# Kernel optimization log

Hardware: AMD Instinct MI355X
Metric: run time of the kernel (lower is better)

The kernel has to match this reference:

```python
import jax, jax.numpy as jnp
import numpy as np

SOFTCLAMP = 50.0
CAUSAL_BLOCK = 256      # causal_block_size (tokens per time block)
NUM_SPECIAL = 8         # num_special_tokens
SPECIAL_SEQ = 2048      # block_size_per_special (defaults to kv seq len)
ROPE_BASE = 10000.0


def setup_inputs() -> dict:
    key = jax.random.key(0)
    kq, kk, kv = jax.random.split(key, 3)
    b, h, hk, s, d = 2, 16, 4, 2048, 64
    q = jax.random.normal(kq, (b, h, s, d), dtype=jnp.float32)
    k = jax.random.normal(kk, (b, hk, s, d), dtype=jnp.float32)
    v = jax.random.normal(kv, (b, hk, s, d), dtype=jnp.float32)
    # standard 1D rotary angles: [seq, dim_head]
    inv_freq = 1.0 / (ROPE_BASE ** (jnp.arange(0, d, 2, dtype=jnp.float32) / d))
    freqs = jnp.arange(s, dtype=jnp.float32)[:, None] * inv_freq[None, :]  # [s, d/2]
    rotations = jnp.concatenate((freqs, freqs), axis=-1)                   # [s, d]
    return {"q": q, "k": k, "v": v, "rotations": rotations}


def _apply_rotations(rotations, t):
    # t: [b, h, s, d]; rotations: [s, d] (broadcast over batch/heads)
    x1, x2 = jnp.split(t, 2, axis=-1)
    rotated_half = jnp.concatenate((-x2, x1), axis=-1)
    return t * jnp.cos(rotations) + rotated_half * jnp.sin(rotations)


def _forward(q, k, v, rotations):
    b, h, i, d = q.shape
    hk, j = k.shape[1], k.shape[2]
    scale = d ** -0.5
    q = _apply_rotations(rotations[:i], q)
    k = _apply_rotations(rotations[:j], k)
    g = h // hk  # GQA groups
    qg = q.reshape(b, hk, g, i, d)
    sim = jnp.einsum('bhgid,bhjd->bhgij', qg, k) * scale
    # softclamp score mod
    sim = jnp.tanh(sim / SOFTCLAMP) * SOFTCLAMP
    # special-token mask (faithful to source: compares raw q/k indices)
    qi = jnp.arange(i)[:, None]
    kj = jnp.arange(j)[None, :]
    special_start = SPECIAL_SEQ - NUM_SPECIAL
    q_is_special = qi >= special_start
    k_is_special = kj >= special_start
    special_mask = ~(~q_is_special & k_is_special)  # non-special q cannot see special k
    # block-causal mask: allowed when query block >= key block
    causal_allow = (qi // CAUSAL_BLOCK) >= (kj // CAUSAL_BLOCK)
    allow = special_mask & causal_allow  # [i, j], broadcasts over b,h,g
    mask_value = -jnp.finfo(sim.dtype).max
    sim = jnp.where(allow, sim, mask_value)
    attn = jax.nn.softmax(sim, axis=-1)
    out = jnp.einsum('bhgij,bhjd->bhgid', attn, v)
    return out.reshape(b, h, i, d)


def reference(q, k, v, rotations):
    return _forward(q, k, v, rotations)
```

## Files before the change

### kernel.cpp

```cpp
#include <hip/hip_runtime.h>
#include <stdint.h>

typedef unsigned short u16;
typedef short s16x8 __attribute__((ext_vector_type(8)));
typedef float f32x4 __attribute__((ext_vector_type(4)));

#define SQ 2048
#define DH 64
#define BN 64
#define STR 72
#define SPECIAL_START 2040
#define NBH 32
#define NKV 8
#define NQP 16
#define NITEMS (NBH * NQP)
#define ATTN_GRID 512
#define K1F  0.18033688011112043f
#define KPAF 4.9244826e-9f
#define KPBF -6.406040185576019e-5f
#define KEF  36.067376022224085f

union U8 { s16x8 v; short e[8]; };
union F4 { f32x4 v; float e[4]; };

__device__ __forceinline__ u16 f2bf(float x) {
    uint32_t u = __float_as_uint(x);
    return (u16)((u + 0x7fffu + ((u >> 16) & 1u)) >> 16);
}
__device__ __forceinline__ uint32_t pkbf(float a, float b) {
    uint32_t r;
    asm("v_cvt_pk_bf16_f32 %0, %1, %2" : "=v"(r) : "v"(a), "v"(b));
    return r;
}
__device__ __forceinline__ float exp2hw(float x) {
    float r; asm("v_exp_f32 %0, %1" : "=v"(r) : "v"(x)); return r;
}
__device__ __forceinline__ float2 fsincos(float ang) {
    float r = ang * 0.15915494309189535f;
    r -= floorf(r);
    float s, c;
    asm("v_sin_f32 %0, %1" : "=v"(s) : "v"(r));
    asm("v_cos_f32 %0, %1" : "=v"(c) : "v"(r));
    return make_float2(s, c);
}
__device__ __forceinline__ void gl_lds16(const void* g, void* l) {
    __builtin_amdgcn_global_load_lds(
        (const __attribute__((address_space(1))) uint32_t*)g,
        (__attribute__((address_space(3))) uint32_t*)l, 16, 0, 0);
}

#define VTILES (NKV * 32)
#define RK (NKV * SQ)
#define KBLK (RK / 32)
__global__ __launch_bounds__(256)
void prep_kernel(const float* __restrict__ kg, const float* __restrict__ vg,
                 const float* __restrict__ rotg,
                 u16* __restrict__ kp, u16* __restrict__ vp,
                 uint32_t* __restrict__ cnt)
{
    const int tid = threadIdx.x;
    if (blockIdx.x == 0 && tid == 0) *cnt = 0u;
    if (blockIdx.x < VTILES) {
        __shared__ short Vls[64 * STR];
        const int tile = blockIdx.x;
        const float* src = vg + ((size_t)(tile >> 5) * SQ + (size_t)(tile & 31) * 64) * DH;
        {
            int kv = tid >> 2, c0 = (tid & 3) * 16;
            const float* s4 = src + (size_t)kv * DH + c0;
            float4 f0 = *(const float4*)(s4);
            float4 f1 = *(const float4*)(s4 + 4);
            float4 f2 = *(const float4*)(s4 + 8);
            float4 f3 = *(const float4*)(s4 + 12);
            uint4 w0 = make_uint4(pkbf(f0.x, f0.y), pkbf(f0.z, f0.w),
                                  pkbf(f1.x, f1.y), pkbf(f1.z, f1.w));
            uint4 w1 = make_uint4(pkbf(f2.x, f2.y), pkbf(f2.z, f2.w),
                                  pkbf(f3.x, f3.y), pkbf(f3.z, f3.w));
            *(uint4*)&Vls[kv * STR + c0]     = w0;
            *(uint4*)&Vls[kv * STR + c0 + 8] = w1;
        }
        __syncthreads();
        {
            int d = tid >> 2, c0 = (tid & 3) * 16;
            U8 o0, o1;
#pragma unroll
            for (int j = 0; j < 16; j++)
                (j < 8 ? o0 : o1).e[j & 7] = Vls[(c0 + j) * STR + d];
            u16* dst = vp + (((size_t)tile * 64 + d) << 6) + c0;
            *(s16x8*)dst       = o0.v;
            *(s16x8*)(dst + 8) = o1.v;
        }
    } else {
        int bx = blockIdx.x - VTILES;
        int r8 = tid >> 3, c0 = (tid & 7) * 4;
        int r = bx * 32 + r8;
        const int s = r & (SQ - 1);
        const float* src = kg + (size_t)r * DH;
        u16*         dst = kp + (size_t)r * DH;
        float4 a  = *(const float4*)(src + c0);
        float4 b  = *(const float4*)(src + c0 + 32);
        float4 rv = *(const float4*)(rotg + (size_t)s * DH + c0);
        float2 s0 = fsincos(rv.x), s1 = fsincos(rv.y),
               s2 = fsincos(rv.z), s3 = fsincos(rv.w);
        float lo0 = a.x * s0.y - b.x * s0.x, hi0 = b.x * s0.y + a.x * s0.x;
        float lo1 = a.y * s1.y - b.y * s1.x, hi1 = b.y * s1.y + a.y * s1.x;
        float lo2 = a.z * s2.y - b.z * s2.x, hi2 = b.z * s2.y + a.z * s2.x;
        float lo3 = a.w * s3.y - b.w * s3.x, hi3 = b.w * s3.y + a.w * s3.x;
        *(uint2*)(dst + c0)      = make_uint2(pkbf(lo0, lo1), pkbf(lo2, lo3));
        *(uint2*)(dst + c0 + 32) = make_uint2(pkbf(hi0, hi1), pkbf(hi2, hi3));
    }
}

__global__ __launch_bounds__(256)
__attribute__((amdgpu_waves_per_eu(3, 4)))
void attn_fast(const float* __restrict__ qg, const float* __restrict__ rotg,
               const u16* __restrict__ kp, const u16* __restrict__ vp,
               uint32_t* __restrict__ cnt, float* __restrict__ outg)
{
    const int tid = threadIdx.x;
    const int wv = tid >> 6, lane = tid & 63;
    const int l15 = lane & 15, quad = lane >> 4;
    const int swl = (l15 & 7) << 3;

    __shared__ __align__(16) u16 Ks[2][4096];
    __shared__ __align__(16) u16 Vt[2][4096];
    __shared__ __align__(16) short Ps[128 * 64];
    __shared__ int s_w;

    const int gcol = (((lane & 7) ^ (lane >> 3)) << 3);
    const int goff0 = ((wv * 16 + (lane >> 3)) << 6) + gcol;
    const int goff1 = goff0 + (8 << 6);
    const int lds0 = (wv * 2) * 512;
    const int lds1 = lds0 + 512;

    short* prow0 = &Ps[(wv * 32 + l15) * 64];
    short* prow1 = &Ps[(wv * 32 + 16 + l15) * 64];

    for (;;) {
        __syncthreads();
        if (tid == 0) s_w = (int)atomicAdd(cnt, 1u);
        __syncthreads();
        const int w = s_w;
        if (w >= NITEMS) break;
        const int qp = (NQP - 1) - (w >> 5);
        const int u  = w & 31, bkv = u >> 2;
        const int bh = ((bkv >> 2) << 4) | ((bkv & 3) << 2) | (u & 3);
        const int nkt = (((qp >> 1) + 1)) << 2;
        const int qrow0 = qp * 128 + wv * 32;

        const u16* kbase = kp + (size_t)bkv * (SQ * DH);
        const u16* vbase = vp + (size_t)bkv * (SQ * DH);
        auto stage = [&](int kt, int cb) {
            const u16* tk = kbase + ((size_t)kt << 12);
            const u16* tv = vbase + ((size_t)kt << 12);
            gl_lds16(tk + goff0, &Ks[cb][lds0]);
            gl_lds16(tk + goff1, &Ks[cb][lds1]);
            gl_lds16(tv + goff0, &Vt[cb][lds0]);
            gl_lds16(tv + goff1, &Vt[cb][lds1]);
        };
        stage(0, 0);

        s16x8 qf[2][2];
#pragma unroll
        for (int nq = 0; nq < 2; nq++) {
            const int srow = qrow0 + nq * 16 + l15;
            const float* gq = qg + ((size_t)bh * SQ + srow) * DH + quad * 8;
            float a[8], b[8];
            *(float4*)&a[0] = *(const float4*)(gq);
            *(float4*)&a[4] = *(const float4*)(gq + 4);
            *(float4*)&b[0] = *(const float4*)(gq + 32);
            *(float4*)&b[4] = *(const float4*)(gq + 36);
            const float* rrow = rotg + (size_t)srow * DH + quad * 8;
            float lo[8], hi[8];
#pragma unroll
            for (int j = 0; j < 8; j++) {
                float2 sc = fsincos(rrow[j]);
                lo[j] = a[j] * sc.y - b[j] * sc.x;
                hi[j] = b[j] * sc.y + a[j] * sc.x;
            }
            U8 q0, q1;
#pragma unroll
            for (int j = 0; j < 4; j++) {
                ((uint32_t*)&q0.v)[j] = pkbf(lo[2 * j], lo[2 * j + 1]);
                ((uint32_t*)&q1.v)[j] = pkbf(hi[2 * j], hi[2 * j + 1]);
            }
            qf[nq][0] = q0.v;
            qf[nq][1] = q1.v;
        }

        F4 oa[2][4];
#pragma unroll
        for (int nq = 0; nq < 2; nq++)
#pragma unroll
            for (int mb = 0; mb < 4; mb++) oa[nq][mb].v = (f32x4){0.f, 0.f, 0.f, 0.f};
        F4 lsa0, lsa1;
        lsa0.v = (f32x4){0.f, 0.f, 0.f, 0.f};
        lsa1.v = (f32x4){0.f, 0.f, 0.f, 0.f};

        __syncthreads();
        int cb = 0;

        for (int kt = 0; kt < nkt; kt++) {
            if (kt + 1 < nkt) stage(kt + 1, cb ^ 1);

            F4 sa[2][4];
            __builtin_amdgcn_s_setprio(1);
#pragma unroll
            for (int ks = 0; ks < 2; ks++)
#pragma unroll
                for (int mb = 0; mb < 4; mb++) {
                    s16x8 kf = *(const s16x8*)&Ks[cb][(mb * 16 + l15) * 64 + ((ks * 32 + quad * 8) ^ swl)];
                    sa[0][mb].v = __builtin_amdgcn_mfma_f32_16x16x32_bf16(
                        kf, qf[0][ks], ks ? sa[0][mb].v : (f32x4){0.f, 0.f, 0.f, 0.f}, 0, 0, 0);
                    sa[1][mb].v = __builtin_amdgcn_mfma_f32_16x16x32_bf16(
                        kf, qf[1][ks], ks ? sa[1][mb].v : (f32x4){0.f, 0.f, 0.f, 0.f}, 0, 0, 0);
                }
            __builtin_amdgcn_s_setprio(0);

            const int last = (kt == 31);
#pragma unroll
            for (int nq = 0; nq < 2; nq++) {
                const int qglob = qrow0 + nq * 16 + l15;
                short* prow = nq ? prow1 : prow0;
#pragma unroll
                for (int mb = 0; mb < 4; mb++) {
                    F4 t, w2, py, pa;
                    t.v  = sa[nq][mb].v * K1F;
                    w2.v = t.v * t.v;
                    py.v = w2.v * KPAF + KPBF;
                    py.v = w2.v * py.v + 1.0f;
                    t.v  = t.v * py.v - KEF;
                    pa.e[0] = exp2hw(t.e[0]);
                    pa.e[1] = exp2hw(t.e[1]);
                    pa.e[2] = exp2hw(t.e[2]);
                    pa.e[3] = exp2hw(t.e[3]);
                    if (last && qglob < SPECIAL_START) {
#pragma unroll
                        for (int c = 0; c < 4; c++) {
                            int kvglob = kt * BN + mb * 16 + quad * 4 + c;
                            if (kvglob >= SPECIAL_START) pa.e[c] = 0.f;
                        }
                    }
                    if (nq) lsa1.v = lsa1.v + pa.v; else lsa0.v = lsa0.v + pa.v;
                    uint2 pw = make_uint2(pkbf(pa.e[0], pa.e[1]),
                                          pkbf(pa.e[2], pa.e[3]));
                    *(uint2*)&prow[(mb * 16 + quad * 4) ^ swl] = pw;
                }
            }

            s16x8 pf00 = *(const s16x8*)&prow0[(quad * 8) ^ swl];
            s16x8 pf01 = *(const s16x8*)&prow0[(32 + quad * 8) ^ swl];
            s16x8 pf10 = *(const s16x8*)&prow1[(quad * 8) ^ swl];
            s16x8 pf11 = *(const s16x8*)&prow1[(32 + quad * 8) ^ swl];
            __builtin_amdgcn_s_setprio(1);
#pragma unroll
            for (int mb = 0; mb < 4; mb++) {
                s16x8 vf = *(const s16x8*)&Vt[cb][(mb * 16 + l15) * 64 + ((quad * 8) ^ swl)];
                oa[0][mb].v = __builtin_amdgcn_mfma_f32_16x16x32_bf16(vf, pf00, oa[0][mb].v, 0, 0, 0);
                oa[1][mb].v = __builtin_amdgcn_mfma_f32_16x16x32_bf16(vf, pf10, oa[1][mb].v, 0, 0, 0);
            }
#pragma unroll
            for (int mb = 0; mb < 4; mb++) {
                s16x8 vf = *(const s16x8*)&Vt[cb][(mb * 16 + l15) * 64 + ((32 + quad * 8) ^ swl)];
                oa[0][mb].v = __builtin_amdgcn_mfma_f32_16x16x32_bf16(vf, pf01, oa[0][mb].v, 0, 0, 0);
                oa[1][mb].v = __builtin_amdgcn_mfma_f32_16x16x32_bf16(vf, pf11, oa[1][mb].v, 0, 0, 0);
            }
            __builtin_amdgcn_s_setprio(0);

            __syncthreads();
            cb ^= 1;
        }

        float lsum0 = (lsa0.e[0] + lsa0.e[1]) + (lsa0.e[2] + lsa0.e[3]);
        float lsum1 = (lsa1.e[0] + lsa1.e[1]) + (lsa1.e[2] + lsa1.e[3]);
        lsum0 += __shfl_xor(lsum0, 16, 64);
        lsum0 += __shfl_xor(lsum0, 32, 64);
        lsum1 += __shfl_xor(lsum1, 16, 64);
        lsum1 += __shfl_xor(lsum1, 32, 64);

#pragma unroll
        for (int nq = 0; nq < 2; nq++) {
            const float rl = 1.0f / (nq ? lsum1 : lsum0);
            const int qrow = qrow0 + nq * 16 + l15;
            float* orow = outg + ((size_t)bh * SQ + qrow) * DH;
#pragma unroll
            for (int mb = 0; mb < 4; mb++) {
                const int d0 = mb * 16 + quad * 4;
                const F4& o = oa[nq][mb];
                *(float4*)(orow + d0) = make_float4(o.e[0] * rl, o.e[1] * rl,
                                                    o.e[2] * rl, o.e[3] * rl);
            }
        }
    }
}

__global__ __launch_bounds__(256, 4)
void attn_fallback(const float* __restrict__ qg, const float* __restrict__ kg,
                   const float* __restrict__ vg, const float* __restrict__ rotg,
                   float* __restrict__ outg)
{
    const int x  = blockIdx.x;
    const int qt = (x & 1) ? (31 - (x >> 1)) : (x >> 1);
    const int bh = blockIdx.y;
    const int bb = bh >> 4, hh = bh & 15;
    const int bkv = bb * 4 + (hh >> 2);
    const int qs = qt * 64;

    const int tid = threadIdx.x;
    const int wv = tid >> 6, lane = tid & 63;
    const int l15 = lane & 15, quad = lane >> 4;
    const int swl = (l15 & 7) << 3;

    __shared__ __align__(16) short QPs[64 * 64];
    __shared__ __align__(16) short Ks[2][BN * 64];
    __shared__ __align__(16) short Vt[2][DH * 64];

    const size_t kvbase = ((size_t)bkv * SQ) * DH;
    const int nkt = (qt / 4 + 1) * 4;
    const int qglob = qs + wv * 16 + l15;

    {
        int rr = tid >> 2, c0 = (tid & 3) * 8;
        int srow = qs + rr;
        const float* gq = qg + ((size_t)bh * SQ + srow) * DH;
        float a[8], b[8];
        *(float4*)&a[0] = *(const float4*)(gq + c0);
        *(float4*)&a[4] = *(const float4*)(gq + c0 + 4);
        *(float4*)&b[0] = *(const float4*)(gq + c0 + 32);
        *(float4*)&b[4] = *(const float4*)(gq + c0 + 36);
        U8 o0, o1;
#pragma unroll
        for (int j = 0; j < 8; j++) {
            float2 sc = fsincos(rotg[(size_t)srow * DH + c0 + j]);
            o0.e[j] = (short)f2bf(a[j] * sc.y - b[j] * sc.x);
            o1.e[j] = (short)f2bf(b[j] * sc.y + a[j] * sc.x);
        }
        int sw2 = (rr & 7) << 3;
        *(s16x8*)&QPs[rr * 64 + (c0 ^ sw2)]        = o0.v;
        *(s16x8*)&QPs[rr * 64 + ((c0 + 32) ^ sw2)] = o1.v;
    }
    __syncthreads();

    s16x8 qf[2];
#pragma unroll
    for (int ks = 0; ks < 2; ks++)
        qf[ks] = *(const s16x8*)&QPs[(wv * 16 + l15) * 64 + ((ks * 32 + quad * 8) ^ swl)];

    F4 oa[4];
#pragma unroll
    for (int mb = 0; mb < 4; mb++) oa[mb].v = (f32x4){0.f, 0.f, 0.f, 0.f};
    float lsum = 0.f;

    for (int kt = 0; kt < nkt; kt++) {
        const int cb = kt & 1;
        {
            int rr = tid >> 2, c0 = (tid & 3) * 8;
            int srow = kt * BN + rr;
            const float* gk = kg + kvbase + (size_t)srow * DH;
            float a[8], b[8];
            *(float4*)&a[0] = *(const float4*)(gk + c0);
            *(float4*)&a[4] = *(const float4*)(gk + c0 + 4);
            *(float4*)&b[0] = *(const float4*)(gk + c0 + 32);
            *(float4*)&b[4] = *(const float4*)(gk + c0 + 36);
            U8 o0, o1;
#pragma unroll
            for (int j = 0; j < 8; j++) {
                float2 sc = fsincos(rotg[(size_t)(srow & (SQ - 1)) * DH + c0 + j]);
                o0.e[j] = (short)f2bf(a[j] * sc.y - b[j] * sc.x);
                o1.e[j] = (short)f2bf(b[j] * sc.y + a[j] * sc.x);
            }
            int sw2 = (rr & 7) << 3;
            *(s16x8*)&Ks[cb][rr * 64 + (c0 ^ sw2)]        = o0.v;
            *(s16x8*)&Ks[cb][rr * 64 + ((c0 + 32) ^ sw2)] = o1.v;
        }
        {
            int rr = tid >> 2, c0 = (tid & 3) * 16;
            const float* gv = vg + kvbase + (size_t)(kt * BN + rr) * DH;
            float vv[16];
#pragma unroll
            for (int t = 0; t < 4; t++)
                *(float4*)&vv[t * 4] = *(const float4*)(gv + c0 + t * 4);
#pragma unroll
            for (int j = 0; j < 16; j++) {
                int d = c0 + j;
                Vt[cb][d * 64 + (rr ^ ((d & 7) << 3))] = (short)f2bf(vv[j]);
            }
        }
        __syncthreads();

        F4 sa[4];
#pragma unroll
        for (int mb = 0; mb < 4; mb++) sa[mb].v = (f32x4){0.f, 0.f, 0.f, 0.f};
#pragma unroll
        for (int ks = 0; ks < 2; ks++)
#pragma unroll
            for (int mb = 0; mb < 4; mb++) {
                s16x8 kf = *(const s16x8*)&Ks[cb][(mb * 16 + l15) * 64 + ((ks * 32 + quad * 8) ^ swl)];
                sa[mb].v = __builtin_amdgcn_mfma_f32_16x16x32_bf16(kf, qf[ks], sa[mb].v, 0, 0, 0);
            }

        F4 pa[4];
#pragma unroll
        for (int mb = 0; mb < 4; mb++)
#pragma unroll
            for (int c = 0; c < 4; c++) {
                float t  = sa[mb].e[c] * K1F;
                float w2 = t * t;
                float poly = fmaf(w2, fmaf(w2, KPAF, KPBF), 1.0f);
                pa[mb].e[c] = exp2hw(fmaf(t, poly, -KEF));
            }
        if (kt == 31 && qglob < SPECIAL_START) {
#pragma unroll
            for (int mb = 0; mb < 4; mb++)
#pragma unroll
                for (int c = 0; c < 4; c++) {
                    int kvglob = kt * BN + mb * 16 + quad * 4 + c;
                    if (kvglob >= SPECIAL_START) pa[mb].e[c] = 0.f;
                }
        }
        short* prow = &QPs[(wv * 16 + l15) * 64];
#pragma unroll
        for (int mb = 0; mb < 4; mb++) {
            lsum += (pa[mb].e[0] + pa[mb].e[1]) + (pa[mb].e[2] + pa[mb].e[3]);
            uint2 pw = make_uint2(pkbf(pa[mb].e[0], pa[mb].e[1]),
                                  pkbf(pa[mb].e[2], pa[mb].e[3]));
            *(uint2*)&prow[(mb * 16 + quad * 4) ^ swl] = pw;
        }
#pragma unroll
        for (int ks = 0; ks < 2; ks++) {
            s16x8 pf = *(const s16x8*)&prow[(ks * 32 + quad * 8) ^ swl];
#pragma unroll
            for (int mb = 0; mb < 4; mb++) {
                s16x8 vf = *(const s16x8*)&Vt[cb][(mb * 16 + l15) * 64 + ((ks * 32 + quad * 8) ^ swl)];
                oa[mb].v = __builtin_amdgcn_mfma_f32_16x16x32_bf16(vf, pf, oa[mb].v, 0, 0, 0);
            }
        }
        __syncthreads();
    }

    lsum += __shfl_xor(lsum, 16, 64);
    lsum += __shfl_xor(lsum, 32, 64);

    float rl = 1.0f / lsum;
    int qrow = qs + wv * 16 + l15;
    float* orow = outg + ((size_t)bh * SQ + qrow) * DH;
#pragma unroll
    for (int mb = 0; mb < 4; mb++) {
        int d0 = mb * 16 + quad * 4;
        *(float4*)(orow + d0) = make_float4(oa[mb].e[0] * rl, oa[mb].e[1] * rl,
                                            oa[mb].e[2] * rl, oa[mb].e[3] * rl);
    }
}

extern "C" void kernel_launch(void* const* d_in, const int* in_sizes, int n_in,
                              void* d_out, int out_size, void* d_ws, size_t ws_size,
                              hipStream_t stream) {
    const float* q   = (const float*)d_in[0];
    const float* k   = (const float*)d_in[1];
    const float* v   = (const float*)d_in[2];
    const float* rot = (const float*)d_in[3];
    float* out = (float*)d_out;

    char* w = (char*)d_ws;
    const size_t k_bytes = (size_t)NKV * SQ * DH * sizeof(u16);
    const size_t v_bytes = k_bytes;
    u16* kp = (u16*)w;
    u16* vp = (u16*)(w + k_bytes);
    uint32_t* cnt = (uint32_t*)(w + k_bytes + v_bytes);

    if (ws_size >= k_bytes + v_bytes + sizeof(uint32_t)) {
        hipLaunchKernelGGL(prep_kernel, dim3(VTILES + KBLK), dim3(256), 0, stream,
                           k, v, rot, kp, vp, cnt);
        hipLaunchKernelGGL(attn_fast, dim3(ATTN_GRID), dim3(256), 0, stream,
                           q, rot, kp, vp, cnt, out);
    } else {
        hipLaunchKernelGGL(attn_fallback, dim3(32, NBH), dim3(256), 0, stream,
                           q, k, v, rot, out);
    }
}
```

Measured before the change: 129.7 us.

## Split long causal query blocks across KV chunks with a separate reduce pass

Work items are now (query-block, KV-range) chunks of up to 8 key tiles, listed in a static table, instead of whole query blocks with variable lengths up to 32 tiles. Each chunk writes unnormalized partial outputs and row sums to workspace, and a new reduce kernel sums the chunks per query block and normalizes. The aim is better load balance and less tail idle time over 768 persistent blocks. In exchange it adds a partial-result write and read through global memory plus an extra kernel launch. The old single-pass kernel is kept as a fallback for small workspaces.

```diff
diff --git a/kernel.cpp b/kernel.cpp
--- a/kernel.cpp
+++ b/kernel.cpp
@@ -13,8 +13,11 @@
 #define NBH 32
 #define NKV 8
 #define NQP 16
-#define NITEMS (NBH * NQP)
-#define ATTN_GRID 512
+#define NCLS 40
+#define NITEMS_F (NCLS * 32)
+#define ATTN_GRID_F 768
+#define NITEMS_M (NBH * NQP)
+#define ATTN_GRID_M 512
 #define K1F  0.18033688011112043f
 #define KPAF 4.9244826e-9f
 #define KPBF -6.406040185576019e-5f
@@ -22,6 +25,32 @@
 
 union U8 { s16x8 v; short e[8]; };
 union F4 { f32x4 v; float e[4]; };
+
+#define CL(qp,k0,nk) ((unsigned short)((qp) | ((k0) << 4) | ((nk) << 9)))
+__device__ const unsigned short ETAB[NCLS] = {
+    CL(15,0,8), CL(15,8,8), CL(15,16,8), CL(15,24,8),
+    CL(14,0,8), CL(14,8,8), CL(14,16,8), CL(14,24,8),
+    CL(13,0,8), CL(13,8,8), CL(13,16,8),
+    CL(12,0,8), CL(12,8,8), CL(12,16,8),
+    CL(11,0,8), CL(11,8,8), CL(11,16,8),
+    CL(10,0,8), CL(10,8,8), CL(10,16,8),
+    CL(9,0,8),  CL(9,8,8),
+    CL(8,0,8),  CL(8,8,8),
+    CL(7,0,8),  CL(7,8,8),
+    CL(6,0,8),  CL(6,8,8),
+    CL(5,0,8),
+    CL(4,0,8),
+    CL(3,0,8),
+    CL(2,0,8),
+    CL(13,24,4), CL(12,24,4), CL(9,16,4), CL(8,16,4),
+    CL(5,8,4),   CL(4,8,4),   CL(1,0,4),  CL(0,0,4)
+};
+__device__ const signed char QPS[16][4] = {
+    {39,-1,-1,-1}, {38,-1,-1,-1}, {31,-1,-1,-1}, {30,-1,-1,-1},
+    {29,37,-1,-1}, {28,36,-1,-1}, {26,27,-1,-1}, {24,25,-1,-1},
+    {22,23,35,-1}, {20,21,34,-1}, {17,18,19,-1}, {14,15,16,-1},
+    {11,12,13,33}, {8,9,10,32},   {4,5,6,7},     {0,1,2,3}
+};
 
 __device__ __forceinline__ u16 f2bf(float x) {
     uint32_t u = __float_as_uint(x);
@@ -114,7 +143,8 @@
 __attribute__((amdgpu_waves_per_eu(3, 4)))
 void attn_fast(const float* __restrict__ qg, const float* __restrict__ rotg,
                const u16* __restrict__ kp, const u16* __restrict__ vp,
-               uint32_t* __restrict__ cnt, float* __restrict__ outg)
+               uint32_t* __restrict__ cnt,
+               float* __restrict__ pacc, float* __restrict__ lacc)
 {
     const int tid = threadIdx.x;
     const int wv = tid >> 6, lane = tid & 63;
@@ -140,11 +170,14 @@
         if (tid == 0) s_w = (int)atomicAdd(cnt, 1u);
         __syncthreads();
         const int w = s_w;
-        if (w >= NITEMS) break;
-        const int qp = (NQP - 1) - (w >> 5);
-        const int u  = w & 31, bkv = u >> 2;
+        if (w >= NITEMS_F) break;
+        const int g = w >> 5;
+        const int u = w & 31, bkv = u >> 2;
         const int bh = ((bkv >> 2) << 4) | ((bkv & 3) << 2) | (u & 3);
-        const int nkt = (((qp >> 1) + 1)) << 2;
+        const int e = ETAB[g];
+        const int qp  = e & 15;
+        const int kt0 = (e >> 4) & 31;
+        const int nk  = e >> 9;
         const int qrow0 = qp * 128 + wv * 32;
 
         const u16* kbase = kp + (size_t)bkv * (SQ * DH);
@@ -157,7 +190,7 @@
             gl_lds16(tv + goff0, &Vt[cb][lds0]);
             gl_lds16(tv + goff1, &Vt[cb][lds1]);
         };
-        stage(0, 0);
+        stage(kt0, 0);
 
         s16x8 qf[2][2];
 #pragma unroll
@@ -199,8 +232,9 @@
         __syncthreads();
         int cb = 0;
 
-        for (int kt = 0; kt < nkt; kt++) {
-            if (kt + 1 < nkt) stage(kt + 1, cb ^ 1);
+        for (int i = 0; i < nk; i++) {
+            const int kt = kt0 + i;
+            if (i + 1 < nk) stage(kt + 1, cb ^ 1);
 
             F4 sa[2][4];
             __builtin_amdgcn_s_setprio(1);
@@ -277,6 +311,229 @@
         lsum1 += __shfl_xor(lsum1, 16, 64);
         lsum1 += __shfl_xor(lsum1, 32, 64);
 
+        float* pitem = pacc + (size_t)w * 8192;
+        float* litem = lacc + (size_t)w * 128;
+#pragma unroll
+        for (int nq = 0; nq < 2; nq++) {
+            const int row = wv * 32 + nq * 16 + l15;
+#pragma unroll
+            for (int mb = 0; mb < 4; mb++) {
+                const F4& o = oa[nq][mb];
+                *(float4*)&pitem[row * 64 + mb * 16 + quad * 4] =
+                    make_float4(o.e[0], o.e[1], o.e[2], o.e[3]);
+            }
+            if (quad == 0) litem[row] = nq ? lsum1 : lsum0;
+        }
+    }
+}
+
+__global__ __launch_bounds__(256)
+void reduce_kernel(const float* __restrict__ pacc, const float* __restrict__ lacc,
+                   float* __restrict__ outg)
+{
+    const int blk = blockIdx.x;
+    const int bh = blk >> 4, qp = blk & 15;
+    const int t = threadIdx.x;
+    const int row = t >> 1;
+    const int c0 = (t & 1) * 32;
+    const int bkv = (bh >> 4) * 4 + ((bh >> 2) & 3);
+    const int u = (bkv << 2) | (bh & 3);
+
+    float acc[32];
+#pragma unroll
+    for (int j = 0; j < 32; j++) acc[j] = 0.f;
+    float ls = 0.f;
+#pragma unroll
+    for (int s = 0; s < 4; s++) {
+        const int g = QPS[qp][s];
+        if (g < 0) break;
+        const int id = g * 32 + u;
+        const float* p = pacc + (size_t)id * 8192 + row * 64 + c0;
+#pragma unroll
+        for (int j = 0; j < 8; j++) {
+            float4 v = ((const float4*)p)[j];
+            acc[4 * j]     += v.x;
+            acc[4 * j + 1] += v.y;
+            acc[4 * j + 2] += v.z;
+            acc[4 * j + 3] += v.w;
+        }
+        ls += lacc[(size_t)id * 128 + row];
+    }
+    const float rl = 1.0f / ls;
+    float* orow = outg + ((size_t)bh * SQ + qp * 128 + row) * DH + c0;
+#pragma unroll
+    for (int j = 0; j < 8; j++)
+        ((float4*)orow)[j] = make_float4(acc[4 * j] * rl, acc[4 * j + 1] * rl,
+                                         acc[4 * j + 2] * rl, acc[4 * j + 3] * rl);
+}
+
+__global__ __launch_bounds__(256)
+__attribute__((amdgpu_waves_per_eu(3, 4)))
+void attn_mid(const float* __restrict__ qg, const float* __restrict__ rotg,
+              const u16* __restrict__ kp, const u16* __restrict__ vp,
+              uint32_t* __restrict__ cnt, float* __restrict__ outg)
+{
+    const int tid = threadIdx.x;
+    const int wv = tid >> 6, lane = tid & 63;
+    const int l15 = lane & 15, quad = lane >> 4;
+    const int swl = (l15 & 7) << 3;
+
+    __shared__ __align__(16) u16 Ks[2][4096];
+    __shared__ __align__(16) u16 Vt[2][4096];
+    __shared__ __align__(16) short Ps[128 * 64];
+    __shared__ int s_w;
+
+    const int gcol = (((lane & 7) ^ (lane >> 3)) << 3);
+    const int goff0 = ((wv * 16 + (lane >> 3)) << 6) + gcol;
+    const int goff1 = goff0 + (8 << 6);
+    const int lds0 = (wv * 2) * 512;
+    const int lds1 = lds0 + 512;
+
+    short* prow0 = &Ps[(wv * 32 + l15) * 64];
+    short* prow1 = &Ps[(wv * 32 + 16 + l15) * 64];
+
+    for (;;) {
+        __syncthreads();
+        if (tid == 0) s_w = (int)atomicAdd(cnt, 1u);
+        __syncthreads();
+        const int w = s_w;
+        if (w >= NITEMS_M) break;
+        const int qp = (NQP - 1) - (w >> 5);
+        const int u  = w & 31, bkv = u >> 2;
+        const int bh = ((bkv >> 2) << 4) | ((bkv & 3) << 2) | (u & 3);
+        const int nkt = (((qp >> 1) + 1)) << 2;
+        const int qrow0 = qp * 128 + wv * 32;
+
+        const u16* kbase = kp + (size_t)bkv * (SQ * DH);
+        const u16* vbase = vp + (size_t)bkv * (SQ * DH);
+        auto stage = [&](int kt, int cb) {
+            const u16* tk = kbase + ((size_t)kt << 12);
+            const u16* tv = vbase + ((size_t)kt << 12);
+            gl_lds16(tk + goff0, &Ks[cb][lds0]);
+            gl_lds16(tk + goff1, &Ks[cb][lds1]);
+            gl_lds16(tv + goff0, &Vt[cb][lds0]);
+            gl_lds16(tv + goff1, &Vt[cb][lds1]);
+        };
+        stage(0, 0);
+
+        s16x8 qf[2][2];
+#pragma unroll
+        for (int nq = 0; nq < 2; nq++) {
+            const int srow = qrow0 + nq * 16 + l15;
+            const float* gq = qg + ((size_t)bh * SQ + srow) * DH + quad * 8;
+            float a[8], b[8];
+            *(float4*)&a[0] = *(const float4*)(gq);
+            *(float4*)&a[4] = *(const float4*)(gq + 4);
+            *(float4*)&b[0] = *(const float4*)(gq + 32);
+            *(float4*)&b[4] = *(const float4*)(gq + 36);
+            const float* rrow = rotg + (size_t)srow * DH + quad * 8;
+            float lo[8], hi[8];
+#pragma unroll
+            for (int j = 0; j < 8; j++) {
+                float2 sc = fsincos(rrow[j]);
+                lo[j] = a[j] * sc.y - b[j] * sc.x;
+                hi[j] = b[j] * sc.y + a[j] * sc.x;
+            }
+            U8 q0, q1;
+#pragma unroll
+            for (int j = 0; j < 4; j++) {
+                ((uint32_t*)&q0.v)[j] = pkbf(lo[2 * j], lo[2 * j + 1]);
+                ((uint32_t*)&q1.v)[j] = pkbf(hi[2 * j], hi[2 * j + 1]);
+            }
+            qf[nq][0] = q0.v;
+            qf[nq][1] = q1.v;
+        }
+
+        F4 oa[2][4];
+#pragma unroll
+        for (int nq = 0; nq < 2; nq++)
+#pragma unroll
+            for (int mb = 0; mb < 4; mb++) oa[nq][mb].v = (f32x4){0.f, 0.f, 0.f, 0.f};
+        F4 lsa0, lsa1;
+        lsa0.v = (f32x4){0.f, 0.f, 0.f, 0.f};
+        lsa1.v = (f32x4){0.f, 0.f, 0.f, 0.f};
+
+        __syncthreads();
+        int cb = 0;
+
+        for (int kt = 0; kt < nkt; kt++) {
+            if (kt + 1 < nkt) stage(kt + 1, cb ^ 1);
+
+            F4 sa[2][4];
+            __builtin_amdgcn_s_setprio(1);
+#pragma unroll
+            for (int ks = 0; ks < 2; ks++)
+#pragma unroll
+                for (int mb = 0; mb < 4; mb++) {
+                    s16x8 kf = *(const s16x8*)&Ks[cb][(mb * 16 + l15) * 64 + ((ks * 32 + quad * 8) ^ swl)];
+                    sa[0][mb].v = __builtin_amdgcn_mfma_f32_16x16x32_bf16(
+                        kf, qf[0][ks], ks ? sa[0][mb].v : (f32x4){0.f, 0.f, 0.f, 0.f}, 0, 0, 0);
+                    sa[1][mb].v = __builtin_amdgcn_mfma_f32_16x16x32_bf16(
+                        kf, qf[1][ks], ks ? sa[1][mb].v : (f32x4){0.f, 0.f, 0.f, 0.f}, 0, 0, 0);
+                }
+            __builtin_amdgcn_s_setprio(0);
+
+            const int last = (kt == 31);
+#pragma unroll
+            for (int nq = 0; nq < 2; nq++) {
+                const int qglob = qrow0 + nq * 16 + l15;
+                short* prow = nq ? prow1 : prow0;
+#pragma unroll
+                for (int mb = 0; mb < 4; mb++) {
+                    F4 t, w2, py, pa;
+                    t.v  = sa[nq][mb].v * K1F;
+                    w2.v = t.v * t.v;
+                    py.v = w2.v * KPAF + KPBF;
+                    py.v = w2.v * py.v + 1.0f;
+                    t.v  = t.v * py.v - KEF;
+                    pa.e[0] = exp2hw(t.e[0]);
+                    pa.e[1] = exp2hw(t.e[1]);
+                    pa.e[2] = exp2hw(t.e[2]);
+                    pa.e[3] = exp2hw(t.e[3]);
+                    if (last && qglob < SPECIAL_START) {
+#pragma unroll
+                        for (int c = 0; c < 4; c++) {
+                            int kvglob = kt * BN + mb * 16 + quad * 4 + c;
+                            if (kvglob >= SPECIAL_START) pa.e[c] = 0.f;
+                        }
+                    }
+                    if (nq) lsa1.v = lsa1.v + pa.v; else lsa0.v = lsa0.v + pa.v;
+                    uint2 pw = make_uint2(pkbf(pa.e[0], pa.e[1]),
+                                          pkbf(pa.e[2], pa.e[3]));
+                    *(uint2*)&prow[(mb * 16 + quad * 4) ^ swl] = pw;
+                }
+            }
+
+            s16x8 pf00 = *(const s16x8*)&prow0[(quad * 8) ^ swl];
+            s16x8 pf01 = *(const s16x8*)&prow0[(32 + quad * 8) ^ swl];
+            s16x8 pf10 = *(const s16x8*)&prow1[(quad * 8) ^ swl];
+            s16x8 pf11 = *(const s16x8*)&prow1[(32 + quad * 8) ^ swl];
+            __builtin_amdgcn_s_setprio(1);
+#pragma unroll
+            for (int mb = 0; mb < 4; mb++) {
+                s16x8 vf = *(const s16x8*)&Vt[cb][(mb * 16 + l15) * 64 + ((quad * 8) ^ swl)];
+                oa[0][mb].v = __builtin_amdgcn_mfma_f32_16x16x32_bf16(vf, pf00, oa[0][mb].v, 0, 0, 0);
+                oa[1][mb].v = __builtin_amdgcn_mfma_f32_16x16x32_bf16(vf, pf10, oa[1][mb].v, 0, 0, 0);
+            }
+#pragma unroll
+            for (int mb = 0; mb < 4; mb++) {
+                s16x8 vf = *(const s16x8*)&Vt[cb][(mb * 16 + l15) * 64 + ((32 + quad * 8) ^ swl)];
+                oa[0][mb].v = __builtin_amdgcn_mfma_f32_16x16x32_bf16(vf, pf01, oa[0][mb].v, 0, 0, 0);
+                oa[1][mb].v = __builtin_amdgcn_mfma_f32_16x16x32_bf16(vf, pf11, oa[1][mb].v, 0, 0, 0);
+            }
+            __builtin_amdgcn_s_setprio(0);
+
+            __syncthreads();
+            cb ^= 1;
+        }
+
+        float lsum0 = (lsa0.e[0] + lsa0.e[1]) + (lsa0.e[2] + lsa0.e[3]);
+        float lsum1 = (lsa1.e[0] + lsa1.e[1]) + (lsa1.e[2] + lsa1.e[3]);
+        lsum0 += __shfl_xor(lsum0, 16, 64);
+        lsum0 += __shfl_xor(lsum0, 32, 64);
+        lsum1 += __shfl_xor(lsum1, 16, 64);
+        lsum1 += __shfl_xor(lsum1, 32, 64);
+
 #pragma unroll
         for (int nq = 0; nq < 2; nq++) {
             const float rl = 1.0f / (nq ? lsum1 : lsum0);
@@ -463,14 +720,30 @@
     char* w = (char*)d_ws;
     const size_t k_bytes = (size_t)NKV * SQ * DH * sizeof(u16);
     const size_t v_bytes = k_bytes;
+    const size_t cnt_off = k_bytes + v_bytes;
+    const size_t pacc_off = cnt_off + 256;
+    const size_t pacc_bytes = (size_t)NITEMS_F * 8192 * sizeof(float);
+    const size_t lacc_off = pacc_off + pacc_bytes;
+    const size_t lacc_bytes = (size_t)NITEMS_F * 128 * sizeof(float);
+    const size_t full_need = lacc_off + lacc_bytes;
+
     u16* kp = (u16*)w;
     u16* vp = (u16*)(w + k_bytes);
-    uint32_t* cnt = (uint32_t*)(w + k_bytes + v_bytes);
-
-    if (ws_size >= k_bytes + v_bytes + sizeof(uint32_t)) {
+    uint32_t* cnt = (uint32_t*)(w + cnt_off);
+    float* pacc = (float*)(w + pacc_off);
+    float* lacc = (float*)(w + lacc_off);
+
+    if (ws_size >= full_need) {
         hipLaunchKernelGGL(prep_kernel, dim3(VTILES + KBLK), dim3(256), 0, stream,
                            k, v, rot, kp, vp, cnt);
-        hipLaunchKernelGGL(attn_fast, dim3(ATTN_GRID), dim3(256), 0, stream,
+        hipLaunchKernelGGL(attn_fast, dim3(ATTN_GRID_F), dim3(256), 0, stream,
+                           q, rot, kp, vp, cnt, pacc, lacc);
+        hipLaunchKernelGGL(reduce_kernel, dim3(NBH * NQP), dim3(256), 0, stream,
+                           pacc, lacc, out);
+    } else if (ws_size >= cnt_off + sizeof(uint32_t)) {
+        hipLaunchKernelGGL(prep_kernel, dim3(VTILES + KBLK), dim3(256), 0, stream,
+                           k, v, rot, kp, vp, cnt);
+        hipLaunchKernelGGL(attn_mid, dim3(ATTN_GRID_M), dim3(256), 0, stream,
                            q, rot, kp, vp, cnt, out);
     } else {
         hipLaunchKernelGGL(attn_fallback, dim3(32, NBH), dim3(256), 0, stream,
```

Measured after the change: 138.8 us. +7.0%, slower.

## Split long query rows across KV chunks with atomic-counted partial merge

Applied to the files above, without the earlier changes.

Work items are redefined through a static table that splits the longer causal query-block rows into chunks of eight key tiles. Partial unnormalised outputs and row sums go to workspace, and the last finisher per query block merges them through an atomic completion counter. V is re-laid out in the prep kernel so each lane loads its MFMA fragments straight from global memory into registers, double-buffered across iterations. This drops the V LDS buffers and allows a larger grid and lower occupancy floor. The aim is better load balance and shorter critical paths, at the cost of extra partial-result traffic, fences and more register pressure.

```diff
diff --git a/kernel.cpp b/kernel.cpp
--- a/kernel.cpp
+++ b/kernel.cpp
@@ -13,8 +13,9 @@
 #define NBH 32
 #define NKV 8
 #define NQP 16
-#define NITEMS (NBH * NQP)
-#define ATTN_GRID 512
+#define NCLS 40
+#define NITEMS_F (NCLS * 32)
+#define ATTN_GRID_F 768
 #define K1F  0.18033688011112043f
 #define KPAF 4.9244826e-9f
 #define KPBF -6.406040185576019e-5f
@@ -22,6 +23,32 @@
 
 union U8 { s16x8 v; short e[8]; };
 union F4 { f32x4 v; float e[4]; };
+
+#define CL(qp,k0,nk,ns) ((unsigned short)((qp) | ((k0) << 4) | ((nk) << 9) | ((ns) << 13)))
+__device__ const unsigned short ETAB[NCLS] = {
+    CL(15,0,8,4), CL(15,8,8,4), CL(15,16,8,4), CL(15,24,8,4),
+    CL(14,0,8,4), CL(14,8,8,4), CL(14,16,8,4), CL(14,24,8,4),
+    CL(13,0,8,4), CL(13,8,8,4), CL(13,16,8,4),
+    CL(12,0,8,4), CL(12,8,8,4), CL(12,16,8,4),
+    CL(11,0,8,3), CL(11,8,8,3), CL(11,16,8,3),
+    CL(10,0,8,3), CL(10,8,8,3), CL(10,16,8,3),
+    CL(9,0,8,3),  CL(9,8,8,3),
+    CL(8,0,8,3),  CL(8,8,8,3),
+    CL(7,0,8,2),  CL(7,8,8,2),
+    CL(6,0,8,2),  CL(6,8,8,2),
+    CL(5,0,8,2),
+    CL(4,0,8,2),
+    CL(3,0,8,1),
+    CL(2,0,8,1),
+    CL(13,24,4,4), CL(12,24,4,4), CL(9,16,4,3), CL(8,16,4,3),
+    CL(5,8,4,2),   CL(4,8,4,2),   CL(1,0,4,1),  CL(0,0,4,1)
+};
+__device__ const signed char QPS[16][4] = {
+    {39,-1,-1,-1}, {38,-1,-1,-1}, {31,-1,-1,-1}, {30,-1,-1,-1},
+    {29,37,-1,-1}, {28,36,-1,-1}, {26,27,-1,-1}, {24,25,-1,-1},
+    {22,23,35,-1}, {20,21,34,-1}, {17,18,19,-1}, {14,15,16,-1},
+    {11,12,13,33}, {8,9,10,32},   {4,5,6,7},     {0,1,2,3}
+};
 
 __device__ __forceinline__ u16 f2bf(float x) {
     uint32_t u = __float_as_uint(x);
@@ -56,10 +83,14 @@
 void prep_kernel(const float* __restrict__ kg, const float* __restrict__ vg,
                  const float* __restrict__ rotg,
                  u16* __restrict__ kp, u16* __restrict__ vp,
-                 uint32_t* __restrict__ cnt)
+                 uint32_t* __restrict__ cnt, uint32_t* __restrict__ done)
 {
     const int tid = threadIdx.x;
-    if (blockIdx.x == 0 && tid == 0) *cnt = 0u;
+    if (blockIdx.x == 0) {
+        if (tid == 0) *cnt = 0u;
+        done[tid] = 0u;
+        done[tid + 256] = 0u;
+    }
     if (blockIdx.x < VTILES) {
         __shared__ short Vls[64 * STR];
         const int tile = blockIdx.x;
@@ -85,9 +116,12 @@
 #pragma unroll
             for (int j = 0; j < 16; j++)
                 (j < 8 ? o0 : o1).e[j & 7] = Vls[(c0 + j) * STR + d];
-            u16* dst = vp + (((size_t)tile * 64 + d) << 6) + c0;
-            *(s16x8*)dst       = o0.v;
-            *(s16x8*)(dst + 8) = o1.v;
+            u16* dst = vp + (size_t)tile * 4096
+                          + ((size_t)((d >> 4) * 2 + (c0 >> 5))) * 512
+                          + (d & 15) * 8;
+            const int q0 = (c0 >> 3) & 3;
+            *(s16x8*)(dst + q0 * 128)       = o0.v;
+            *(s16x8*)(dst + (q0 + 1) * 128) = o1.v;
         }
     } else {
         int bx = blockIdx.x - VTILES;
@@ -111,10 +145,12 @@
 }
 
 __global__ __launch_bounds__(256)
-__attribute__((amdgpu_waves_per_eu(3, 4)))
+__attribute__((amdgpu_waves_per_eu(2, 4)))
 void attn_fast(const float* __restrict__ qg, const float* __restrict__ rotg,
                const u16* __restrict__ kp, const u16* __restrict__ vp,
-               uint32_t* __restrict__ cnt, float* __restrict__ outg)
+               uint32_t* __restrict__ cnt, uint32_t* __restrict__ done,
+               float* __restrict__ pacc, float* __restrict__ lacc,
+               float* __restrict__ outg)
 {
     const int tid = threadIdx.x;
     const int wv = tid >> 6, lane = tid & 63;
@@ -122,9 +158,8 @@
     const int swl = (l15 & 7) << 3;
 
     __shared__ __align__(16) u16 Ks[2][4096];
-    __shared__ __align__(16) u16 Vt[2][4096];
     __shared__ __align__(16) short Ps[128 * 64];
-    __shared__ int s_w;
+    __shared__ int s_w, s_d;
 
     const int gcol = (((lane & 7) ^ (lane >> 3)) << 3);
     const int goff0 = ((wv * 16 + (lane >> 3)) << 6) + gcol;
@@ -140,24 +175,33 @@
         if (tid == 0) s_w = (int)atomicAdd(cnt, 1u);
         __syncthreads();
         const int w = s_w;
-        if (w >= NITEMS) break;
-        const int qp = (NQP - 1) - (w >> 5);
-        const int u  = w & 31, bkv = u >> 2;
+        if (w >= NITEMS_F) break;
+        const int g = w >> 5;
+        const int u = w & 31, bkv = u >> 2;
         const int bh = ((bkv >> 2) << 4) | ((bkv & 3) << 2) | (u & 3);
-        const int nkt = (((qp >> 1) + 1)) << 2;
+        const int e = ETAB[g];
+        const int qp  = e & 15;
+        const int kt0 = (e >> 4) & 31;
+        const int nk  = (e >> 9) & 15;
+        const int nsl = e >> 13;
         const int qrow0 = qp * 128 + wv * 32;
 
         const u16* kbase = kp + (size_t)bkv * (SQ * DH);
-        const u16* vbase = vp + (size_t)bkv * (SQ * DH);
-        auto stage = [&](int kt, int cb) {
+        const u16* vbase = vp + ((size_t)(bkv * 32)) * 4096 + lane * 8;
+        auto stage_k = [&](int kt, int cb) {
             const u16* tk = kbase + ((size_t)kt << 12);
-            const u16* tv = vbase + ((size_t)kt << 12);
             gl_lds16(tk + goff0, &Ks[cb][lds0]);
             gl_lds16(tk + goff1, &Ks[cb][lds1]);
-            gl_lds16(tv + goff0, &Vt[cb][lds0]);
-            gl_lds16(tv + goff1, &Vt[cb][lds1]);
         };
-        stage(0, 0);
+        s16x8 vfA[8], vfB[8];
+        auto loadV = [&](s16x8 (&vf)[8], int kt) {
+            const u16* p = vbase + ((size_t)kt << 12);
+#pragma unroll
+            for (int f = 0; f < 8; f++)
+                vf[f] = *(const s16x8*)(p + f * 512);
+        };
+        stage_k(kt0, 0);
+        loadV(vfA, kt0);
 
         s16x8 qf[2][2];
 #pragma unroll
@@ -195,14 +239,9 @@
         F4 lsa0, lsa1;
         lsa0.v = (f32x4){0.f, 0.f, 0.f, 0.f};
         lsa1.v = (f32x4){0.f, 0.f, 0.f, 0.f};
-
-        __syncthreads();
-        int cb = 0;
-
-        for (int kt = 0; kt < nkt; kt++) {
-            if (kt + 1 < nkt) stage(kt + 1, cb ^ 1);
-
-            F4 sa[2][4];
+        F4 sa[2][4];
+
+        auto QK = [&](int cb) {
             __builtin_amdgcn_s_setprio(1);
 #pragma unroll
             for (int ks = 0; ks < 2; ks++)
@@ -215,7 +254,8 @@
                         kf, qf[1][ks], ks ? sa[1][mb].v : (f32x4){0.f, 0.f, 0.f, 0.f}, 0, 0, 0);
                 }
             __builtin_amdgcn_s_setprio(0);
-
+        };
+        auto SM = [&](int kt) {
             const int last = (kt == 31);
 #pragma unroll
             for (int nq = 0; nq < 2; nq++) {
@@ -246,7 +286,8 @@
                     *(uint2*)&prow[(mb * 16 + quad * 4) ^ swl] = pw;
                 }
             }
-
+        };
+        auto PV = [&](const s16x8 (&vf)[8]) {
             s16x8 pf00 = *(const s16x8*)&prow0[(quad * 8) ^ swl];
             s16x8 pf01 = *(const s16x8*)&prow0[(32 + quad * 8) ^ swl];
             s16x8 pf10 = *(const s16x8*)&prow1[(quad * 8) ^ swl];
@@ -254,20 +295,34 @@
             __builtin_amdgcn_s_setprio(1);
 #pragma unroll
             for (int mb = 0; mb < 4; mb++) {
-                s16x8 vf = *(const s16x8*)&Vt[cb][(mb * 16 + l15) * 64 + ((quad * 8) ^ swl)];
-                oa[0][mb].v = __builtin_amdgcn_mfma_f32_16x16x32_bf16(vf, pf00, oa[0][mb].v, 0, 0, 0);
-                oa[1][mb].v = __builtin_amdgcn_mfma_f32_16x16x32_bf16(vf, pf10, oa[1][mb].v, 0, 0, 0);
+                oa[0][mb].v = __builtin_amdgcn_mfma_f32_16x16x32_bf16(vf[mb * 2], pf00, oa[0][mb].v, 0, 0, 0);
+                oa[1][mb].v = __builtin_amdgcn_mfma_f32_16x16x32_bf16(vf[mb * 2], pf10, oa[1][mb].v, 0, 0, 0);
             }
 #pragma unroll
             for (int mb = 0; mb < 4; mb++) {
-                s16x8 vf = *(const s16x8*)&Vt[cb][(mb * 16 + l15) * 64 + ((32 + quad * 8) ^ swl)];
-                oa[0][mb].v = __builtin_amdgcn_mfma_f32_16x16x32_bf16(vf, pf01, oa[0][mb].v, 0, 0, 0);
-                oa[1][mb].v = __builtin_amdgcn_mfma_f32_16x16x32_bf16(vf, pf11, oa[1][mb].v, 0, 0, 0);
+                oa[0][mb].v = __builtin_amdgcn_mfma_f32_16x16x32_bf16(vf[mb * 2 + 1], pf01, oa[0][mb].v, 0, 0, 0);
+                oa[1][mb].v = __builtin_amdgcn_mfma_f32_16x16x32_bf16(vf[mb * 2 + 1], pf11, oa[1][mb].v, 0, 0, 0);
             }
             __builtin_amdgcn_s_setprio(0);
-
-            __syncthreads();
-            cb ^= 1;
+        };
+
+        __syncthreads();
+        int cb = 0;
+
+        for (int i = 0; i < nk; i += 2) {
+            const int kt = kt0 + i;
+            stage_k(kt + 1, cb ^ 1);
+            QK(cb);
+            loadV(vfB, kt + 1);
+            SM(kt);
+            PV(vfA);
+            __syncthreads(); cb ^= 1;
+            if (i + 2 < nk) stage_k(kt + 2, cb ^ 1);
+            QK(cb);
+            if (i + 2 < nk) loadV(vfA, kt + 2);
+            SM(kt + 1);
+            PV(vfB);
+            __syncthreads(); cb ^= 1;
         }
 
         float lsum0 = (lsa0.e[0] + lsa0.e[1]) + (lsa0.e[2] + lsa0.e[3]);
@@ -277,17 +332,72 @@
         lsum1 += __shfl_xor(lsum1, 16, 64);
         lsum1 += __shfl_xor(lsum1, 32, 64);
 
-#pragma unroll
-        for (int nq = 0; nq < 2; nq++) {
-            const float rl = 1.0f / (nq ? lsum1 : lsum0);
-            const int qrow = qrow0 + nq * 16 + l15;
-            float* orow = outg + ((size_t)bh * SQ + qrow) * DH;
-#pragma unroll
-            for (int mb = 0; mb < 4; mb++) {
-                const int d0 = mb * 16 + quad * 4;
-                const F4& o = oa[nq][mb];
-                *(float4*)(orow + d0) = make_float4(o.e[0] * rl, o.e[1] * rl,
-                                                    o.e[2] * rl, o.e[3] * rl);
+        if (nsl == 1) {
+#pragma unroll
+            for (int nq = 0; nq < 2; nq++) {
+                const float rl = 1.0f / (nq ? lsum1 : lsum0);
+                const int qrow = qrow0 + nq * 16 + l15;
+                float* orow = outg + ((size_t)bh * SQ + qrow) * DH;
+#pragma unroll
+                for (int mb = 0; mb < 4; mb++) {
+                    const int d0 = mb * 16 + quad * 4;
+                    const F4& o = oa[nq][mb];
+                    *(float4*)(orow + d0) = make_float4(o.e[0] * rl, o.e[1] * rl,
+                                                        o.e[2] * rl, o.e[3] * rl);
+                }
+            }
+        } else {
+            float* pitem = pacc + (size_t)w * 8192;
+            float* litem = lacc + (size_t)w * 128;
+#pragma unroll
+            for (int nq = 0; nq < 2; nq++) {
+                const int row = wv * 32 + nq * 16 + l15;
+#pragma unroll
+                for (int mb = 0; mb < 4; mb++) {
+                    const F4& o = oa[nq][mb];
+                    *(float4*)&pitem[row * 64 + mb * 16 + quad * 4] =
+                        make_float4(o.e[0], o.e[1], o.e[2], o.e[3]);
+                }
+                if (quad == 0) litem[row] = nq ? lsum1 : lsum0;
+            }
+            __threadfence();
+            __syncthreads();
+            if (tid == 0) s_d = (int)atomicAdd(&done[bh * 16 + qp], 1u);
+            __syncthreads();
+            if (s_d == nsl - 1) {
+                __threadfence();
+#pragma unroll
+                for (int s = 0; s < 4; s++) {
+                    const int g2 = QPS[qp][s];
+                    if (g2 < 0 || g2 == g) continue;
+                    const size_t id = (size_t)g2 * 32 + u;
+                    const float* pp = pacc + id * 8192;
+                    const float* lp = lacc + id * 128;
+#pragma unroll
+                    for (int nq = 0; nq < 2; nq++) {
+                        const int row = wv * 32 + nq * 16 + l15;
+#pragma unroll
+                        for (int mb = 0; mb < 4; mb++) {
+                            float4 v = *(const float4*)&pp[row * 64 + mb * 16 + quad * 4];
+                            F4& o = oa[nq][mb];
+                            o.e[0] += v.x; o.e[1] += v.y; o.e[2] += v.z; o.e[3] += v.w;
+                        }
+                        if (nq) lsum1 += lp[row]; else lsum0 += lp[row];
+                    }
+                }
+#pragma unroll
+                for (int nq = 0; nq < 2; nq++) {
+                    const float rl = 1.0f / (nq ? lsum1 : lsum0);
+                    const int qrow = qrow0 + nq * 16 + l15;
+                    float* orow = outg + ((size_t)bh * SQ + qrow) * DH;
+#pragma unroll
+                    for (int mb = 0; mb < 4; mb++) {
+                        const int d0 = mb * 16 + quad * 4;
+                        const F4& o = oa[nq][mb];
+                        *(float4*)(orow + d0) = make_float4(o.e[0] * rl, o.e[1] * rl,
+                                                            o.e[2] * rl, o.e[3] * rl);
+                    }
+                }
             }
         }
     }
@@ -463,15 +573,21 @@
     char* w = (char*)d_ws;
     const size_t k_bytes = (size_t)NKV * SQ * DH * sizeof(u16);
     const size_t v_bytes = k_bytes;
+    size_t off = k_bytes + v_bytes;
+    uint32_t* cnt  = (uint32_t*)(w + off); off += 256;
+    uint32_t* done = (uint32_t*)(w + off); off += 4096;
+    float* pacc = (float*)(w + off); off += (size_t)NITEMS_F * 8192 * sizeof(float);
+    float* lacc = (float*)(w + off); off += (size_t)NITEMS_F * 128 * sizeof(float);
+    const size_t full_need = off;
+
     u16* kp = (u16*)w;
     u16* vp = (u16*)(w + k_bytes);
-    uint32_t* cnt = (uint32_t*)(w + k_bytes + v_bytes);
-
-    if (ws_size >= k_bytes + v_bytes + sizeof(uint32_t)) {
+
+    if (ws_size >= full_need) {
         hipLaunchKernelGGL(prep_kernel, dim3(VTILES + KBLK), dim3(256), 0, stream,
-                           k, v, rot, kp, vp, cnt);
-        hipLaunchKernelGGL(attn_fast, dim3(ATTN_GRID), dim3(256), 0, stream,
-                           q, rot, kp, vp, cnt, out);
+                           k, v, rot, kp, vp, cnt, done);
+        hipLaunchKernelGGL(attn_fast, dim3(ATTN_GRID_F), dim3(256), 0, stream,
+                           q, rot, kp, vp, cnt, done, pacc, lacc, out);
     } else {
         hipLaunchKernelGGL(attn_fallback, dim3(32, NBH), dim3(256), 0, stream,
                            q, k, v, rot, out);
```

Measured after the change: 322.7 us. +148.8%, slower.
